# Performance work log

Measured on AMD Instinct MI355X. Metric: run time of the kernel, lower is better.

Reference implementation:

```python
import jax, jax.numpy as jnp
import numpy as np

N = 64      # num_agents
Z = 512     # z_dim
D = 512     # d_model


def setup_inputs() -> dict:
    key = jax.random.key(0)
    k0, k1, k2, k3, k4 = jax.random.split(key, 5)
    z = jax.random.normal(k0, (N, Z), dtype=jnp.float32)
    # per-agent unshared projections (bias=False), kaiming-uniform-ish scale
    s = 1.0 / np.sqrt(Z).astype(np.float32)
    Wq = jax.random.normal(k1, (N, D, Z), dtype=jnp.float32) * s
    Wk = jax.random.normal(k2, (N, D, Z), dtype=jnp.float32) * s
    Wv = jax.random.normal(k3, (N, D, Z), dtype=jnp.float32) * s
    Wi = jax.random.normal(k4, (Z, D), dtype=jnp.float32) * (1.0 / np.sqrt(D).astype(np.float32))
    bi = jnp.zeros((Z,), dtype=jnp.float32)
    return {"z": z, "Wq": Wq, "Wk": Wk, "Wv": Wv, "Wi": Wi, "bi": bi}


def reference(z, Wq, Wk, Wv, Wi, bi):
    n, d = z.shape[0], Wq.shape[1]
    scale = jnp.sqrt(jnp.asarray(d, z.dtype))
    # batched per-agent GEMV: Q[n] = Wq[n] @ z[n]
    Q = jnp.einsum('ndz,nz->nd', Wq, z)
    K = jnp.einsum('ndz,nz->nd', Wk, z)
    V = jnp.einsum('ndz,nz->nd', Wv, z)
    # S[i, j] = <K_i, Q_j> / sqrt(d); complete graph minus self-edges
    S = (K @ Q.T) / scale
    S = jnp.where(jnp.eye(n, dtype=bool), -jnp.inf, S)
    alpha = jax.nn.softmax(S, axis=0)            # softmax over senders i for each receiver j
    messages = jnp.einsum('ij,id->jd', alpha, V)  # (N, D)
    # infer aux loss: each sender i is inferred identically by all N-1 receivers,
    # so the mean over N*(N-1) pairs equals the mean over i of per-agent MSE.
    hat = V @ Wi.T + bi                           # (N, Z)
    per_agent_mse = jnp.mean((hat - z) ** 2, axis=1)
    total_infer_loss = jnp.mean(per_agent_mse)
    return messages, total_infer_loss
```

## Files before the change

### kernel.cpp

```cpp
#include <hip/hip_runtime.h>
#include <math.h>

#define NAG 64
#define ZD  512
#define DM  512

__global__ __launch_bounds__(256) void qkv_gemv_kernel(
    const float* __restrict__ z,
    const float* __restrict__ Wq,
    const float* __restrict__ Wk,
    const float* __restrict__ Wv,
    float* __restrict__ Q, float* __restrict__ K, float* __restrict__ V)
{
    const int wave = threadIdx.x >> 6;
    const int lane = threadIdx.x & 63;
    const int rowBase = blockIdx.x * 16 + wave * 4;
    const int m   = rowBase >> 15;
    const int rem = rowBase & 32767;
    const int n   = rem >> 9;
    const int d0  = rem & 511;

    const float* __restrict__ W = (m == 0) ? Wq : ((m == 1) ? Wk : Wv);
    float* __restrict__ O       = (m == 0) ? Q  : ((m == 1) ? K  : V);

    const float* zr = z + n * ZD;
    const float4 zA = *reinterpret_cast<const float4*>(zr + lane * 4);
    const float4 zB = *reinterpret_cast<const float4*>(zr + 256 + lane * 4);

    const float* Wbase = W + ((size_t)(n * DM + d0)) * ZD;
    float acc[4];
#pragma unroll
    for (int r = 0; r < 4; ++r) {
        const float* wr = Wbase + (size_t)r * ZD;
        const float4 a = *reinterpret_cast<const float4*>(wr + lane * 4);
        const float4 b = *reinterpret_cast<const float4*>(wr + 256 + lane * 4);
        acc[r] = a.x*zA.x + a.y*zA.y + a.z*zA.z + a.w*zA.w
               + b.x*zB.x + b.y*zB.y + b.z*zB.z + b.w*zB.w;
    }
#pragma unroll
    for (int r = 0; r < 4; ++r) {
        float v = acc[r];
#pragma unroll
        for (int off = 32; off > 0; off >>= 1) v += __shfl_down(v, off);
        if (lane == 0) O[n * DM + d0 + r] = v;
    }
}

__global__ __launch_bounds__(256) void attn_msg_kernel(
    const float* __restrict__ Q, const float* __restrict__ K,
    const float* __restrict__ V, float* __restrict__ out)
{
    __shared__ __align__(16) float Qs[DM];
    __shared__ float Sc[NAG];
    __shared__ float Al[NAG];
    const int j = blockIdx.x;
    const int t = threadIdx.x;

    Qs[t]       = Q[j * DM + t];
    Qs[t + 256] = Q[j * DM + t + 256];
    __syncthreads();

    const int i = t >> 2;
    const int c = t & 3;
    const float* Krow = K + i * DM + c * 128;
    const float* Qsub = Qs + c * 128;
    float p = 0.f;
#pragma unroll
    for (int k = 0; k < 32; ++k) {
        float4 kv = *reinterpret_cast<const float4*>(Krow + k * 4);
        float4 qv = *reinterpret_cast<const float4*>(Qsub + k * 4);
        p += kv.x*qv.x + kv.y*qv.y + kv.z*qv.z + kv.w*qv.w;
    }
    p += __shfl_xor(p, 1);
    p += __shfl_xor(p, 2);
    if (c == 0) {
        Sc[i] = (i == j) ? -INFINITY : p * 0.044194173824159216f;
    }
    __syncthreads();

    if (t < 64) {
        float s = Sc[t];
        float mx = s;
#pragma unroll
        for (int off = 32; off > 0; off >>= 1) mx = fmaxf(mx, __shfl_xor(mx, off));
        float e = expf(s - mx);
        float sum = e;
#pragma unroll
        for (int off = 32; off > 0; off >>= 1) sum += __shfl_xor(sum, off);
        Al[t] = e / sum;
    }
    __syncthreads();

#pragma unroll
    for (int dd = 0; dd < 2; ++dd) {
        const int d = t + dd * 256;
        float acc = 0.f;
        for (int i2 = 0; i2 < NAG; ++i2) acc += Al[i2] * V[i2 * DM + d];
        out[j * DM + d] = acc;
    }
}

__global__ __launch_bounds__(256) void infer_loss_kernel(
    const float* __restrict__ V, const float* __restrict__ Wi,
    const float* __restrict__ bi, const float* __restrict__ z,
    float* __restrict__ zp_partial)
{
    __shared__ __align__(16) float Ws[DM];
    __shared__ float wsum[4];
    const int zp = blockIdx.x;
    const int t  = threadIdx.x;

    const float* wr = Wi + (size_t)zp * DM;
    Ws[t]       = wr[t];
    Ws[t + 256] = wr[t + 256];
    __syncthreads();

    const int i = t >> 2;
    const int c = t & 3;
    const float* Vrow = V + i * DM + c * 128;
    const float* Wsub = Ws + c * 128;
    float p = 0.f;
#pragma unroll
    for (int k = 0; k < 32; ++k) {
        float4 vv = *reinterpret_cast<const float4*>(Vrow + k * 4);
        float4 wv = *reinterpret_cast<const float4*>(Wsub + k * 4);
        p += vv.x*wv.x + vv.y*wv.y + vv.z*wv.z + vv.w*wv.w;
    }
    p += __shfl_xor(p, 1);
    p += __shfl_xor(p, 2);

    float e2 = 0.f;
    if (c == 0) {
        float e = p + bi[zp] - z[i * ZD + zp];
        e2 = e * e;
    }
#pragma unroll
    for (int off = 32; off > 0; off >>= 1) e2 += __shfl_down(e2, off);

    const int wave = t >> 6;
    const int lane = t & 63;
    if (lane == 0) wsum[wave] = e2;
    __syncthreads();
    if (t == 0) zp_partial[zp] = wsum[0] + wsum[1] + wsum[2] + wsum[3];
}

__global__ __launch_bounds__(64) void loss_reduce_kernel(
    const float* __restrict__ zp_partial, float* __restrict__ out)
{
    float v = 0.f;
#pragma unroll
    for (int k = 0; k < 8; ++k) v += zp_partial[threadIdx.x + k * 64];
#pragma unroll
    for (int off = 32; off > 0; off >>= 1) v += __shfl_down(v, off);
    if (threadIdx.x == 0) out[NAG * DM] = v * (1.0f / (NAG * ZD));
}

extern "C" void kernel_launch(void* const* d_in, const int* in_sizes, int n_in,
                              void* d_out, int out_size, void* d_ws, size_t ws_size,
                              hipStream_t stream) {
    const float* z  = (const float*)d_in[0];
    const float* Wq = (const float*)d_in[1];
    const float* Wk = (const float*)d_in[2];
    const float* Wv = (const float*)d_in[3];
    const float* Wi = (const float*)d_in[4];
    const float* bi = (const float*)d_in[5];
    float* out = (float*)d_out;

    float* Q = (float*)d_ws;
    float* K = Q + NAG * DM;
    float* V = K + NAG * DM;
    float* partial = V + NAG * DM;

    hipLaunchKernelGGL(qkv_gemv_kernel, dim3(6144), dim3(256), 0, stream,
                       z, Wq, Wk, Wv, Q, K, V);
    hipLaunchKernelGGL(attn_msg_kernel, dim3(NAG), dim3(256), 0, stream,
                       Q, K, V, out);
    hipLaunchKernelGGL(infer_loss_kernel, dim3(ZD), dim3(256), 0, stream,
                       V, Wi, bi, z, partial);
    hipLaunchKernelGGL(loss_reduce_kernel, dim3(1), dim3(64), 0, stream,
                       partial, out);
}
```

Measured before the change: 53.95 us.

## Software-pipeline QKV GEMV loads across row groups and merge attention/loss kernels

```diff
diff --git a/kernel.cpp b/kernel.cpp
--- a/kernel.cpp
+++ b/kernel.cpp
@@ -4,6 +4,65 @@
 #define NAG 64
 #define ZD  512
 #define DM  512
+
+struct GBuf {
+    float4 w0, w1, w2, w3, w4, w5, w6, w7;
+    float4 zA, zB;
+    float* outp;
+};
+
+__device__ __forceinline__ void issue_group(
+    int rowBase, int lane,
+    const float* __restrict__ z,
+    const float* __restrict__ Wq, const float* __restrict__ Wk,
+    const float* __restrict__ Wv,
+    float* __restrict__ Q, float* __restrict__ K, float* __restrict__ V,
+    GBuf& b)
+{
+    const int m   = rowBase >> 15;
+    const int rem = rowBase & 32767;
+    const int n   = rem >> 9;
+    const int d0  = rem & 511;
+    const float* __restrict__ W = (m == 0) ? Wq : ((m == 1) ? Wk : Wv);
+    float* __restrict__ O       = (m == 0) ? Q  : ((m == 1) ? K  : V);
+
+    const float* zr = z + n * ZD;
+    b.zA = *reinterpret_cast<const float4*>(zr + lane * 4);
+    b.zB = *reinterpret_cast<const float4*>(zr + 256 + lane * 4);
+
+    const float* Wb = W + ((size_t)(n * DM + d0)) * ZD;
+    b.w0 = *reinterpret_cast<const float4*>(Wb + lane * 4);
+    b.w1 = *reinterpret_cast<const float4*>(Wb + 256 + lane * 4);
+    b.w2 = *reinterpret_cast<const float4*>(Wb + ZD + lane * 4);
+    b.w3 = *reinterpret_cast<const float4*>(Wb + ZD + 256 + lane * 4);
+    b.w4 = *reinterpret_cast<const float4*>(Wb + 2 * ZD + lane * 4);
+    b.w5 = *reinterpret_cast<const float4*>(Wb + 2 * ZD + 256 + lane * 4);
+    b.w6 = *reinterpret_cast<const float4*>(Wb + 3 * ZD + lane * 4);
+    b.w7 = *reinterpret_cast<const float4*>(Wb + 3 * ZD + 256 + lane * 4);
+    b.outp = O + n * DM + d0;
+}
+
+__device__ __forceinline__ void compute_group(int lane, const GBuf& b)
+{
+    float a0 = b.w0.x*b.zA.x + b.w0.y*b.zA.y + b.w0.z*b.zA.z + b.w0.w*b.zA.w
+             + b.w1.x*b.zB.x + b.w1.y*b.zB.y + b.w1.z*b.zB.z + b.w1.w*b.zB.w;
+    float a1 = b.w2.x*b.zA.x + b.w2.y*b.zA.y + b.w2.z*b.zA.z + b.w2.w*b.zA.w
+             + b.w3.x*b.zB.x + b.w3.y*b.zB.y + b.w3.z*b.zB.z + b.w3.w*b.zB.w;
+    float a2 = b.w4.x*b.zA.x + b.w4.y*b.zA.y + b.w4.z*b.zA.z + b.w4.w*b.zA.w
+             + b.w5.x*b.zB.x + b.w5.y*b.zB.y + b.w5.z*b.zB.z + b.w5.w*b.zB.w;
+    float a3 = b.w6.x*b.zA.x + b.w6.y*b.zA.y + b.w6.z*b.zA.z + b.w6.w*b.zA.w
+             + b.w7.x*b.zB.x + b.w7.y*b.zB.y + b.w7.z*b.zB.z + b.w7.w*b.zB.w;
+#pragma unroll
+    for (int off = 32; off > 0; off >>= 1) {
+        a0 += __shfl_down(a0, off);
+        a1 += __shfl_down(a1, off);
+        a2 += __shfl_down(a2, off);
+        a3 += __shfl_down(a3, off);
+    }
+    if (lane == 0) {
+        b.outp[0] = a0; b.outp[1] = a1; b.outp[2] = a2; b.outp[3] = a3;
+    }
+}
 
 __global__ __launch_bounds__(256) void qkv_gemv_kernel(
     const float* __restrict__ z,
@@ -14,134 +73,107 @@
 {
     const int wave = threadIdx.x >> 6;
     const int lane = threadIdx.x & 63;
-    const int rowBase = blockIdx.x * 16 + wave * 4;
-    const int m   = rowBase >> 15;
-    const int rem = rowBase & 32767;
-    const int n   = rem >> 9;
-    const int d0  = rem & 511;
-
-    const float* __restrict__ W = (m == 0) ? Wq : ((m == 1) ? Wk : Wv);
-    float* __restrict__ O       = (m == 0) ? Q  : ((m == 1) ? K  : V);
-
-    const float* zr = z + n * ZD;
-    const float4 zA = *reinterpret_cast<const float4*>(zr + lane * 4);
-    const float4 zB = *reinterpret_cast<const float4*>(zr + 256 + lane * 4);
-
-    const float* Wbase = W + ((size_t)(n * DM + d0)) * ZD;
-    float acc[4];
-#pragma unroll
-    for (int r = 0; r < 4; ++r) {
-        const float* wr = Wbase + (size_t)r * ZD;
-        const float4 a = *reinterpret_cast<const float4*>(wr + lane * 4);
-        const float4 b = *reinterpret_cast<const float4*>(wr + 256 + lane * 4);
-        acc[r] = a.x*zA.x + a.y*zA.y + a.z*zA.z + a.w*zA.w
-               + b.x*zB.x + b.y*zB.y + b.z*zB.z + b.w*zB.w;
-    }
-#pragma unroll
-    for (int r = 0; r < 4; ++r) {
-        float v = acc[r];
-#pragma unroll
-        for (int off = 32; off > 0; off >>= 1) v += __shfl_down(v, off);
-        if (lane == 0) O[n * DM + d0 + r] = v;
-    }
-}
-
-__global__ __launch_bounds__(256) void attn_msg_kernel(
+    const int gw = blockIdx.x * 4 + wave;
+    const int rb = gw * 12;
+
+    GBuf A, B;
+    issue_group(rb,     lane, z, Wq, Wk, Wv, Q, K, V, A);
+    issue_group(rb + 4, lane, z, Wq, Wk, Wv, Q, K, V, B);
+    compute_group(lane, A);
+    issue_group(rb + 8, lane, z, Wq, Wk, Wv, Q, K, V, A);
+    compute_group(lane, B);
+    compute_group(lane, A);
+}
+
+__global__ __launch_bounds__(256) void attn_infer_kernel(
     const float* __restrict__ Q, const float* __restrict__ K,
-    const float* __restrict__ V, float* __restrict__ out)
-{
-    __shared__ __align__(16) float Qs[DM];
+    const float* __restrict__ V, const float* __restrict__ Wi,
+    const float* __restrict__ bi, const float* __restrict__ z,
+    float* __restrict__ out, float* __restrict__ zp_partial)
+{
+    __shared__ __align__(16) float sbuf[DM];
     __shared__ float Sc[NAG];
     __shared__ float Al[NAG];
-    const int j = blockIdx.x;
     const int t = threadIdx.x;
 
-    Qs[t]       = Q[j * DM + t];
-    Qs[t + 256] = Q[j * DM + t + 256];
-    __syncthreads();
-
-    const int i = t >> 2;
-    const int c = t & 3;
-    const float* Krow = K + i * DM + c * 128;
-    const float* Qsub = Qs + c * 128;
-    float p = 0.f;
-#pragma unroll
-    for (int k = 0; k < 32; ++k) {
-        float4 kv = *reinterpret_cast<const float4*>(Krow + k * 4);
-        float4 qv = *reinterpret_cast<const float4*>(Qsub + k * 4);
-        p += kv.x*qv.x + kv.y*qv.y + kv.z*qv.z + kv.w*qv.w;
+    if (blockIdx.x < NAG) {
+        const int j = blockIdx.x;
+        sbuf[t]       = Q[j * DM + t];
+        sbuf[t + 256] = Q[j * DM + t + 256];
+        __syncthreads();
+
+        const int i = t >> 2;
+        const int c = t & 3;
+        const float* Krow = K + i * DM + c * 128;
+        const float* Qsub = sbuf + c * 128;
+        float p = 0.f;
+#pragma unroll
+        for (int k = 0; k < 32; ++k) {
+            float4 kv = *reinterpret_cast<const float4*>(Krow + k * 4);
+            float4 qv = *reinterpret_cast<const float4*>(Qsub + k * 4);
+            p += kv.x*qv.x + kv.y*qv.y + kv.z*qv.z + kv.w*qv.w;
+        }
+        p += __shfl_xor(p, 1);
+        p += __shfl_xor(p, 2);
+        if (c == 0)
+            Sc[i] = (i == j) ? -INFINITY : p * 0.044194173824159216f;
+        __syncthreads();
+
+        if (t < 64) {
+            float s = Sc[t];
+            float mx = s;
+#pragma unroll
+            for (int off = 32; off > 0; off >>= 1) mx = fmaxf(mx, __shfl_xor(mx, off));
+            float e = expf(s - mx);
+            float sum = e;
+#pragma unroll
+            for (int off = 32; off > 0; off >>= 1) sum += __shfl_xor(sum, off);
+            Al[t] = e / sum;
+        }
+        __syncthreads();
+
+#pragma unroll
+        for (int dd = 0; dd < 2; ++dd) {
+            const int d = t + dd * 256;
+            float acc = 0.f;
+            for (int i2 = 0; i2 < NAG; ++i2) acc += Al[i2] * V[i2 * DM + d];
+            out[j * DM + d] = acc;
+        }
+    } else {
+        const int zp = blockIdx.x - NAG;
+        const float* wr = Wi + (size_t)zp * DM;
+        sbuf[t]       = wr[t];
+        sbuf[t + 256] = wr[t + 256];
+        __syncthreads();
+
+        const int i = t >> 2;
+        const int c = t & 3;
+        const float* Vrow = V + i * DM + c * 128;
+        const float* Wsub = sbuf + c * 128;
+        float p = 0.f;
+#pragma unroll
+        for (int k = 0; k < 32; ++k) {
+            float4 vv = *reinterpret_cast<const float4*>(Vrow + k * 4);
+            float4 wv = *reinterpret_cast<const float4*>(Wsub + k * 4);
+            p += vv.x*wv.x + vv.y*wv.y + vv.z*wv.z + vv.w*wv.w;
+        }
+        p += __shfl_xor(p, 1);
+        p += __shfl_xor(p, 2);
+
+        float e2 = 0.f;
+        if (c == 0) {
+            float e = p + bi[zp] - z[i * ZD + zp];
+            e2 = e * e;
+        }
+#pragma unroll
+        for (int off = 32; off > 0; off >>= 1) e2 += __shfl_down(e2, off);
+
+        const int wv2 = t >> 6;
+        const int ln  = t & 63;
+        if (ln == 0) Sc[wv2] = e2;
+        __syncthreads();
+        if (t == 0) zp_partial[zp] = Sc[0] + Sc[1] + Sc[2] + Sc[3];
     }
-    p += __shfl_xor(p, 1);
-    p += __shfl_xor(p, 2);
-    if (c == 0) {
-        Sc[i] = (i == j) ? -INFINITY : p * 0.044194173824159216f;
-    }
-    __syncthreads();
-
-    if (t < 64) {
-        float s = Sc[t];
-        float mx = s;
-#pragma unroll
-        for (int off = 32; off > 0; off >>= 1) mx = fmaxf(mx, __shfl_xor(mx, off));
-        float e = expf(s - mx);
-        float sum = e;
-#pragma unroll
-        for (int off = 32; off > 0; off >>= 1) sum += __shfl_xor(sum, off);
-        Al[t] = e / sum;
-    }
-    __syncthreads();
-
-#pragma unroll
-    for (int dd = 0; dd < 2; ++dd) {
-        const int d = t + dd * 256;
-        float acc = 0.f;
-        for (int i2 = 0; i2 < NAG; ++i2) acc += Al[i2] * V[i2 * DM + d];
-        out[j * DM + d] = acc;
-    }
-}
-
-__global__ __launch_bounds__(256) void infer_loss_kernel(
-    const float* __restrict__ V, const float* __restrict__ Wi,
-    const float* __restrict__ bi, const float* __restrict__ z,
-    float* __restrict__ zp_partial)
-{
-    __shared__ __align__(16) float Ws[DM];
-    __shared__ float wsum[4];
-    const int zp = blockIdx.x;
-    const int t  = threadIdx.x;
-
-    const float* wr = Wi + (size_t)zp * DM;
-    Ws[t]       = wr[t];
-    Ws[t + 256] = wr[t + 256];
-    __syncthreads();
-
-    const int i = t >> 2;
-    const int c = t & 3;
-    const float* Vrow = V + i * DM + c * 128;
-    const float* Wsub = Ws + c * 128;
-    float p = 0.f;
-#pragma unroll
-    for (int k = 0; k < 32; ++k) {
-        float4 vv = *reinterpret_cast<const float4*>(Vrow + k * 4);
-        float4 wv = *reinterpret_cast<const float4*>(Wsub + k * 4);
-        p += vv.x*wv.x + vv.y*wv.y + vv.z*wv.z + vv.w*wv.w;
-    }
-    p += __shfl_xor(p, 1);
-    p += __shfl_xor(p, 2);
-
-    float e2 = 0.f;
-    if (c == 0) {
-        float e = p + bi[zp] - z[i * ZD + zp];
-        e2 = e * e;
-    }
-#pragma unroll
-    for (int off = 32; off > 0; off >>= 1) e2 += __shfl_down(e2, off);
-
-    const int wave = t >> 6;
-    const int lane = t & 63;
-    if (lane == 0) wsum[wave] = e2;
-    __syncthreads();
-    if (t == 0) zp_partial[zp] = wsum[0] + wsum[1] + wsum[2] + wsum[3];
 }
 
 __global__ __launch_bounds__(64) void loss_reduce_kernel(
@@ -171,12 +203,10 @@
     float* V = K + NAG * DM;
     float* partial = V + NAG * DM;
 
-    hipLaunchKernelGGL(qkv_gemv_kernel, dim3(6144), dim3(256), 0, stream,
+    hipLaunchKernelGGL(qkv_gemv_kernel, dim3(2048), dim3(256), 0, stream,
                        z, Wq, Wk, Wv, Q, K, V);
-    hipLaunchKernelGGL(attn_msg_kernel, dim3(NAG), dim3(256), 0, stream,
-                       Q, K, V, out);
-    hipLaunchKernelGGL(infer_loss_kernel, dim3(ZD), dim3(256), 0, stream,
-                       V, Wi, bi, z, partial);
+    hipLaunchKernelGGL(attn_infer_kernel, dim3(NAG + ZD), dim3(256), 0, stream,
+                       Q, K, V, Wi, bi, z, out, partial);
     hipLaunchKernelGGL(loss_reduce_kernel, dim3(1), dim3(64), 0, stream,
                        partial, out);
 }
```

Measured after the change: 52.28 us. 1.03x faster.

## Fuse attention and infer-loss kernels with last-block reduction, nontemporal weight loads

Applied to the files above, without the earlier changes.

```diff
diff --git a/kernel.cpp b/kernel.cpp
--- a/kernel.cpp
+++ b/kernel.cpp
@@ -4,6 +4,8 @@
 #define NAG 64
 #define ZD  512
 #define DM  512
+
+typedef float f32x4 __attribute__((ext_vector_type(4)));
 
 __global__ __launch_bounds__(256) void qkv_gemv_kernel(
     const float* __restrict__ z,
@@ -24,135 +26,141 @@
     float* __restrict__ O       = (m == 0) ? Q  : ((m == 1) ? K  : V);
 
     const float* zr = z + n * ZD;
-    const float4 zA = *reinterpret_cast<const float4*>(zr + lane * 4);
-    const float4 zB = *reinterpret_cast<const float4*>(zr + 256 + lane * 4);
+    const f32x4 zA = *reinterpret_cast<const f32x4*>(zr + lane * 4);
+    const f32x4 zB = *reinterpret_cast<const f32x4*>(zr + 256 + lane * 4);
 
     const float* Wbase = W + ((size_t)(n * DM + d0)) * ZD;
     float acc[4];
 #pragma unroll
     for (int r = 0; r < 4; ++r) {
         const float* wr = Wbase + (size_t)r * ZD;
-        const float4 a = *reinterpret_cast<const float4*>(wr + lane * 4);
-        const float4 b = *reinterpret_cast<const float4*>(wr + 256 + lane * 4);
-        acc[r] = a.x*zA.x + a.y*zA.y + a.z*zA.z + a.w*zA.w
-               + b.x*zB.x + b.y*zB.y + b.z*zB.z + b.w*zB.w;
+        const f32x4 a = __builtin_nontemporal_load(
+            reinterpret_cast<const f32x4*>(wr + lane * 4));
+        const f32x4 b = __builtin_nontemporal_load(
+            reinterpret_cast<const f32x4*>(wr + 256 + lane * 4));
+        acc[r] = a[0]*zA[0] + a[1]*zA[1] + a[2]*zA[2] + a[3]*zA[3]
+               + b[0]*zB[0] + b[1]*zB[1] + b[2]*zB[2] + b[3]*zB[3];
     }
+    float a0 = acc[0], a1 = acc[1], a2 = acc[2], a3 = acc[3];
 #pragma unroll
-    for (int r = 0; r < 4; ++r) {
-        float v = acc[r];
-#pragma unroll
-        for (int off = 32; off > 0; off >>= 1) v += __shfl_down(v, off);
-        if (lane == 0) O[n * DM + d0 + r] = v;
+    for (int off = 32; off > 0; off >>= 1) {
+        a0 += __shfl_down(a0, off);
+        a1 += __shfl_down(a1, off);
+        a2 += __shfl_down(a2, off);
+        a3 += __shfl_down(a3, off);
     }
+    if (lane == 0)
+        *reinterpret_cast<float4*>(O + n * DM + d0) = make_float4(a0, a1, a2, a3);
 }
 
-__global__ __launch_bounds__(256) void attn_msg_kernel(
+__global__ __launch_bounds__(256) void attn_infer_kernel(
     const float* __restrict__ Q, const float* __restrict__ K,
-    const float* __restrict__ V, float* __restrict__ out)
+    const float* __restrict__ V, const float* __restrict__ Wi,
+    const float* __restrict__ bi, const float* __restrict__ z,
+    float* __restrict__ out, float* __restrict__ zp_partial,
+    unsigned int* __restrict__ counter)
 {
-    __shared__ __align__(16) float Qs[DM];
+    __shared__ __align__(16) float sbuf[DM];
     __shared__ float Sc[NAG];
     __shared__ float Al[NAG];
-    const int j = blockIdx.x;
+    __shared__ int is_last;
     const int t = threadIdx.x;
 
-    Qs[t]       = Q[j * DM + t];
-    Qs[t + 256] = Q[j * DM + t + 256];
-    __syncthreads();
+    if (blockIdx.x < NAG) {
+        const int j = blockIdx.x;
+        sbuf[t]       = Q[j * DM + t];
+        sbuf[t + 256] = Q[j * DM + t + 256];
+        __syncthreads();
 
-    const int i = t >> 2;
-    const int c = t & 3;
-    const float* Krow = K + i * DM + c * 128;
-    const float* Qsub = Qs + c * 128;
-    float p = 0.f;
+        const int i = t >> 2;
+        const int c = t & 3;
+        const float* Krow = K + i * DM + c * 128;
+        const float* Qsub = sbuf + c * 128;
+        float p = 0.f;
 #pragma unroll
-    for (int k = 0; k < 32; ++k) {
-        float4 kv = *reinterpret_cast<const float4*>(Krow + k * 4);
-        float4 qv = *reinterpret_cast<const float4*>(Qsub + k * 4);
-        p += kv.x*qv.x + kv.y*qv.y + kv.z*qv.z + kv.w*qv.w;
-    }
-    p += __shfl_xor(p, 1);
-    p += __shfl_xor(p, 2);
-    if (c == 0) {
-        Sc[i] = (i == j) ? -INFINITY : p * 0.044194173824159216f;
-    }
-    __syncthreads();
+        for (int k = 0; k < 32; ++k) {
+            float4 kv = *reinterpret_cast<const float4*>(Krow + k * 4);
+            float4 qv = *reinterpret_cast<const float4*>(Qsub + k * 4);
+            p += kv.x*qv.x + kv.y*qv.y + kv.z*qv.z + kv.w*qv.w;
+        }
+        p += __shfl_xor(p, 1);
+        p += __shfl_xor(p, 2);
+        if (c == 0)
+            Sc[i] = (i == j) ? -INFINITY : p * 0.044194173824159216f;
+        __syncthreads();
 
-    if (t < 64) {
-        float s = Sc[t];
-        float mx = s;
+        if (t < 64) {
+            float s = Sc[t];
+            float mx = s;
 #pragma unroll
-        for (int off = 32; off > 0; off >>= 1) mx = fmaxf(mx, __shfl_xor(mx, off));
-        float e = expf(s - mx);
-        float sum = e;
+            for (int off = 32; off > 0; off >>= 1) mx = fmaxf(mx, __shfl_xor(mx, off));
+            float e = expf(s - mx);
+            float sum = e;
 #pragma unroll
-        for (int off = 32; off > 0; off >>= 1) sum += __shfl_xor(sum, off);
-        Al[t] = e / sum;
-    }
-    __syncthreads();
+            for (int off = 32; off > 0; off >>= 1) sum += __shfl_xor(sum, off);
+            Al[t] = e / sum;
+        }
+        __syncthreads();
 
 #pragma unroll
-    for (int dd = 0; dd < 2; ++dd) {
-        const int d = t + dd * 256;
-        float acc = 0.f;
-        for (int i2 = 0; i2 < NAG; ++i2) acc += Al[i2] * V[i2 * DM + d];
-        out[j * DM + d] = acc;
+        for (int dd = 0; dd < 2; ++dd) {
+            const int d = t + dd * 256;
+            float acc = 0.f;
+            for (int i2 = 0; i2 < NAG; ++i2) acc += Al[i2] * V[i2 * DM + d];
+            out[j * DM + d] = acc;
+        }
+    } else {
+        const int zp = blockIdx.x - NAG;
+        const float* wr = Wi + (size_t)zp * DM;
+        sbuf[t]       = wr[t];
+        sbuf[t + 256] = wr[t + 256];
+        __syncthreads();
+
+        const int i = t >> 2;
+        const int c = t & 3;
+        const float* Vrow = V + i * DM + c * 128;
+        const float* Wsub = sbuf + c * 128;
+        float p = 0.f;
+#pragma unroll
+        for (int k = 0; k < 32; ++k) {
+            float4 vv = *reinterpret_cast<const float4*>(Vrow + k * 4);
+            float4 wv = *reinterpret_cast<const float4*>(Wsub + k * 4);
+            p += vv.x*wv.x + vv.y*wv.y + vv.z*wv.z + vv.w*wv.w;
+        }
+        p += __shfl_xor(p, 1);
+        p += __shfl_xor(p, 2);
+
+        float e2 = 0.f;
+        if (c == 0) {
+            float e = p + bi[zp] - z[i * ZD + zp];
+            e2 = e * e;
+        }
+#pragma unroll
+        for (int off = 32; off > 0; off >>= 1) e2 += __shfl_down(e2, off);
+
+        const int wv2 = t >> 6;
+        const int ln  = t & 63;
+        if (ln == 0) Sc[wv2] = e2;
+        __syncthreads();
+        if (t == 0) {
+            zp_partial[zp] = Sc[0] + Sc[1] + Sc[2] + Sc[3];
+            __threadfence();
+            unsigned int old = atomicAdd(counter, 1u);
+            is_last = (old == ZD - 1);
+        }
+        __syncthreads();
+
+        if (is_last && t < 64) {
+            __threadfence();
+            volatile const float* vp = zp_partial;
+            float v = 0.f;
+#pragma unroll
+            for (int k = 0; k < 8; ++k) v += vp[t + k * 64];
+#pragma unroll
+            for (int off = 32; off > 0; off >>= 1) v += __shfl_down(v, off);
+            if (t == 0) out[NAG * DM] = v * (1.0f / (NAG * ZD));
+        }
     }
-}
-
-__global__ __launch_bounds__(256) void infer_loss_kernel(
-    const float* __restrict__ V, const float* __restrict__ Wi,
-    const float* __restrict__ bi, const float* __restrict__ z,
-    float* __restrict__ zp_partial)
-{
-    __shared__ __align__(16) float Ws[DM];
-    __shared__ float wsum[4];
-    const int zp = blockIdx.x;
-    const int t  = threadIdx.x;
-
-    const float* wr = Wi + (size_t)zp * DM;
-    Ws[t]       = wr[t];
-    Ws[t + 256] = wr[t + 256];
-    __syncthreads();
-
-    const int i = t >> 2;
-    const int c = t & 3;
-    const float* Vrow = V + i * DM + c * 128;
-    const float* Wsub = Ws + c * 128;
-    float p = 0.f;
-#pragma unroll
-    for (int k = 0; k < 32; ++k) {
-        float4 vv = *reinterpret_cast<const float4*>(Vrow + k * 4);
-        float4 wv = *reinterpret_cast<const float4*>(Wsub + k * 4);
-        p += vv.x*wv.x + vv.y*wv.y + vv.z*wv.z + vv.w*wv.w;
-    }
-    p += __shfl_xor(p, 1);
-    p += __shfl_xor(p, 2);
-
-    float e2 = 0.f;
-    if (c == 0) {
-        float e = p + bi[zp] - z[i * ZD + zp];
-        e2 = e * e;
-    }
-#pragma unroll
-    for (int off = 32; off > 0; off >>= 1) e2 += __shfl_down(e2, off);
-
-    const int wave = t >> 6;
-    const int lane = t & 63;
-    if (lane == 0) wsum[wave] = e2;
-    __syncthreads();
-    if (t == 0) zp_partial[zp] = wsum[0] + wsum[1] + wsum[2] + wsum[3];
-}
-
-__global__ __launch_bounds__(64) void loss_reduce_kernel(
-    const float* __restrict__ zp_partial, float* __restrict__ out)
-{
-    float v = 0.f;
-#pragma unroll
-    for (int k = 0; k < 8; ++k) v += zp_partial[threadIdx.x + k * 64];
-#pragma unroll
-    for (int off = 32; off > 0; off >>= 1) v += __shfl_down(v, off);
-    if (threadIdx.x == 0) out[NAG * DM] = v * (1.0f / (NAG * ZD));
 }
 
 extern "C" void kernel_launch(void* const* d_in, const int* in_sizes, int n_in,
@@ -170,13 +178,12 @@
     float* K = Q + NAG * DM;
     float* V = K + NAG * DM;
     float* partial = V + NAG * DM;
+    unsigned int* counter = (unsigned int*)(partial + ZD);
+
+    (void)hipMemsetAsync(counter, 0, sizeof(unsigned int), stream);
 
     hipLaunchKernelGGL(qkv_gemv_kernel, dim3(6144), dim3(256), 0, stream,
                        z, Wq, Wk, Wv, Q, K, V);
-    hipLaunchKernelGGL(attn_msg_kernel, dim3(NAG), dim3(256), 0, stream,
-                       Q, K, V, out);
-    hipLaunchKernelGGL(infer_loss_kernel, dim3(ZD), dim3(256), 0, stream,
-                       V, Wi, bi, z, partial);
-    hipLaunchKernelGGL(loss_reduce_kernel, dim3(1), dim3(64), 0, stream,
-                       partial, out);
+    hipLaunchKernelGGL(attn_infer_kernel, dim3(NAG + ZD), dim3(256), 0, stream,
+                       Q, K, V, Wi, bi, z, out, partial, counter);
 }
```

Result: slower. 65.57 us (+21.5%).
